# Kernel tuning notes

Measured on AMD Instinct MI355X. Metric: run time of the kernel, lower is better.

The kernel has to match this reference:

```python
import jax, jax.numpy as jnp
import numpy as np

N, E, D, H, O, L = 50000, 400000, 128, 128, 64, 2


def setup_inputs() -> dict:
    key = jax.random.key(0)
    ks = jax.random.split(key, 24)
    s = 0.05
    rn = lambda k, shape: jax.random.normal(k, shape, jnp.float32) * s
    # random edges with no self-loops (dst = src + nonzero offset mod N)
    src = jax.random.randint(ks[0], (E,), 0, N, dtype=jnp.int32)
    off = jax.random.randint(ks[1], (E,), 1, N, dtype=jnp.int32)
    dst = (src + off) % N
    edge_index = jnp.stack([src, dst])  # [2, E] int32
    return {
        "x": rn(ks[2], (N, D)),
        "edge_index": edge_index,
        "attn_W": rn(ks[3], (L, 2 * D, 2)),
        "attn_b": rn(ks[4], (L, 2)),
        "mlp_W1": rn(ks[5], (L, D, H)),
        "mlp_b1": rn(ks[6], (L, H)),
        "mlp_W2": rn(ks[7], (L, H, H)),
        "mlp_b2": rn(ks[8], (L, H)),
        "bn_gamma": jnp.ones((L, H), jnp.float32),   # torch BatchNorm1d default affine init
        "bn_beta": jnp.zeros((L, H), jnp.float32),
        "gru_Wih": rn(ks[9], (D, 3 * H)),
        "gru_Whh": rn(ks[10], (H, 3 * H)),
        "gru_bih": rn(ks[11], (3 * H,)),
        "gru_bhh": rn(ks[12], (3 * H,)),
        "last_W1": rn(ks[13], (H, H)),
        "last_b1": rn(ks[14], (H,)),
        "last_W2": rn(ks[15], (H, O)),
        "last_b2": rn(ks[16], (O,)),
    }


def reference(x, edge_index, attn_W, attn_b, mlp_W1, mlp_b1, mlp_W2, mlp_b2,
              bn_gamma, bn_beta, gru_Wih, gru_Whh, gru_bih, gru_bhh,
              last_W1, last_b1, last_W2, last_b2):
    n = x.shape[0]
    # symmetrize edge list: message (nbr -> node) for both directions
    node = jnp.concatenate([edge_index[0], edge_index[1]])  # destination
    nbr = jnp.concatenate([edge_index[1], edge_index[0]])   # source / neighbor
    deg = jax.ops.segment_sum(jnp.ones((node.shape[0], 1), x.dtype), node, num_segments=n)
    has_nbr = deg > 0

    h_state = jnp.zeros((n, gru_Whh.shape[0]), x.dtype)
    for l in range(attn_W.shape[0]):
        feats = x[nbr]  # [2E, d] gather
        s_agg = jax.ops.segment_sum(feats, node, num_segments=n)
        m_agg = jax.ops.segment_max(feats, node, num_segments=n)
        m_agg = jnp.where(has_nbr, m_agg, jnp.zeros_like(m_agg))  # isolated nodes stay 0
        # attention over {sum, max} aggregations
        scores = jnp.concatenate([s_agg, m_agg], axis=1) @ attn_W[l] + attn_b[l]  # [n, 2]
        w = jax.nn.softmax(scores, axis=1)
        comb = x + w[:, :1] * s_agg + w[:, 1:] * m_agg
        # MLP (in -> hidden, ReLU, hidden -> out)
        z = jax.nn.relu(comb @ mlp_W1[l] + mlp_b1[l]) @ mlp_W2[l] + mlp_b2[l]
        # BatchNorm1d in eval mode with running stats (mean 0, var 1): affine only
        z = z * bn_gamma[l] + bn_beta[l]
        # GRUCell
        gi = z @ gru_Wih + gru_bih
        gh = h_state @ gru_Whh + gru_bhh
        ir, iz, inn = jnp.split(gi, 3, axis=1)
        hr, hz, hn = jnp.split(gh, 3, axis=1)
        r = jax.nn.sigmoid(ir + hr)
        u = jax.nn.sigmoid(iz + hz)
        ncand = jnp.tanh(inn + r * hn)
        h_state = (1.0 - u) * ncand + u * h_state
        x = h_state
    # final node-level MLP
    out = jax.nn.relu(x @ last_W1 + last_b1) @ last_W2 + last_b2
    return out
```

## Files before the change

### kernel.cpp

```cpp
#include <hip/hip_runtime.h>
#include <math.h>

typedef unsigned short u16;
typedef __attribute__((ext_vector_type(8))) short bf16x8;
typedef __attribute__((ext_vector_type(4))) float f32x4;

#define ADJ_CAP 96

__device__ __forceinline__ u16 f2b(float f) {
    union { float f; unsigned u; } v; v.f = f;
    unsigned r = (v.u + 0x7FFF + ((v.u >> 16) & 1)) >> 16;
    return (u16)r;
}
__device__ __forceinline__ float b2f(u16 h) {
    union { unsigned u; float f; } v; v.u = (unsigned)h << 16;
    return v.f;
}
__device__ __forceinline__ float u2f(unsigned u) {
    union { unsigned u; float f; } v; v.u = u;
    return v.f;
}
__device__ __forceinline__ float fsig(float x) { return 1.f / (1.f + __expf(-x)); }
__device__ __forceinline__ float ftanh(float x) {
    float e = __expf(2.f * x);
    return 1.f - 2.f / (e + 1.f);
}

__device__ __forceinline__ void gll16(const void* g, void* l) {
    __builtin_amdgcn_global_load_lds(
        (const __attribute__((address_space(1))) void*)g,
        (__attribute__((address_space(3))) void*)l, 16, 0, 0);
}

__device__ __forceinline__ void conv_chunk(const float* __restrict__ src,
                                           u16* __restrict__ dst, int c, int NC) {
    int sl = c / NC, n = c - sl * NC;
    u16 tmp[8];
#pragma unroll
    for (int i = 0; i < 8; ++i) tmp[i] = f2b(src[(size_t)(sl * 8 + i) * NC + n]);
    *(uint4*)(dst + (size_t)c * 8) = *(const uint4*)tmp;
}

__global__ void k_pro(const int* __restrict__ ei, int* __restrict__ cnt,
                      u16* __restrict__ adj, int E, int N,
                      const float* __restrict__ W1, const float* __restrict__ W2,
                      const float* __restrict__ Wih, const float* __restrict__ Whh,
                      const float* __restrict__ lW1, const float* __restrict__ lW2,
                      u16* __restrict__ tW1, u16* __restrict__ tW2,
                      u16* __restrict__ tGRU,
                      u16* __restrict__ tlW1, u16* __restrict__ tlW2, int L,
                      const float* __restrict__ x, u16* __restrict__ xb, int n8) {
    const int EB = (E + 255) >> 8;
    const int nwc = L * 4096 + 12288 + 3072;
    const int WB = (nwc + 255) >> 8;
    int b = blockIdx.x;
    if (b < EB * 8) {
        const int part = b & 7, chunk = b >> 3;
        const int span = (N + 7) >> 3;
        const int nlo = part * span;
        const int nhi = (nlo + span < N) ? nlo + span : N;
        int e = chunk * 256 + threadIdx.x;
        if (e < E) {
            int s = ei[e], d = ei[E + e];
            if (s >= nlo && s < nhi) {
                int p = atomicAdd(&cnt[s], 1);
                adj[(size_t)s * ADJ_CAP + p] = (u16)d;
            }
            if (d >= nlo && d < nhi) {
                int q = atomicAdd(&cnt[d], 1);
                adj[(size_t)d * ADJ_CAP + q] = (u16)s;
            }
        }
        return;
    }
    b -= EB * 8;
    if (b < WB) {
        int c = b * 256 + threadIdx.x;
        if (c >= nwc) return;
        if (c < L * 2048) { int l = c >> 11; conv_chunk(W1 + (size_t)l * 16384, tW1 + (size_t)l * 16384, c & 2047, 128); return; }
        c -= L * 2048;
        if (c < L * 2048) { int l = c >> 11; conv_chunk(W2 + (size_t)l * 16384, tW2 + (size_t)l * 16384, c & 2047, 128); return; }
        c -= L * 2048;
        if (c < 12288) {
            int s = c >> 9, r = c & 511;
            int q = r >> 7, mat = (r >> 6) & 1, cc = r & 63;
            int h = s / 12, s2 = s % 12, kc = s2 / 3, g = s2 % 3;
            int ocol = g * 128 + h * 64 + cc;
            const float* src = mat ? Whh : Wih;
            int kb = (kc * 4 + q) * 8;
            u16 tmp[8];
#pragma unroll
            for (int e = 0; e < 8; ++e) tmp[e] = f2b(src[(size_t)(kb + e) * 384 + ocol]);
            *(uint4*)(tGRU + (size_t)c * 8) = *(const uint4*)tmp;
            return;
        }
        c -= 12288;
        if (c < 2048) { conv_chunk(lW1, tlW1, c, 128); return; }
        c -= 2048;
        if (c < 1024) { conv_chunk(lW2, tlW2, c, 64); return; }
        return;
    }
    b -= WB;
    {
        int i = b * 256 + threadIdx.x;
        if (i < n8) {
            float4 a = *(const float4*)(x + (size_t)i * 8);
            float4 bb = *(const float4*)(x + (size_t)i * 8 + 4);
            u16 t[8] = {f2b(a.x), f2b(a.y), f2b(a.z), f2b(a.w),
                        f2b(bb.x), f2b(bb.y), f2b(bb.z), f2b(bb.w)};
            *(uint4*)(xb + (size_t)i * 8) = *(const uint4*)t;
        }
    }
}

__global__ __launch_bounds__(256) void k_agg(const u16* __restrict__ xb,
                                             const u16* __restrict__ adj,
                                             const int* __restrict__ cnt,
                                             const float* __restrict__ aW,
                                             const float* __restrict__ ab,
                                             u16* __restrict__ comb, int N) {
    int n = blockIdx.x * 4 + (threadIdx.x >> 6);
    if (n >= N) return;
    int l = threadIdx.x & 63;
    int grp = l >> 4;
    int f0 = (l & 15) * 8;
    int beg = n * ADJ_CAP, deg = cnt[n], end = beg + deg;
    float s[8], m[8];
#pragma unroll
    for (int i = 0; i < 8; ++i) { s[i] = 0.f; m[i] = -3.402823e38f; }

    auto acc8 = [&](uint4 v) {
        unsigned d[4] = {v.x, v.y, v.z, v.w};
#pragma unroll
        for (int i = 0; i < 4; ++i) {
            float a0 = u2f(d[i] << 16);
            float a1 = u2f(d[i] & 0xFFFF0000u);
            s[2 * i] += a0;     m[2 * i] = fmaxf(m[2 * i], a0);
            s[2 * i + 1] += a1; m[2 * i + 1] = fmaxf(m[2 * i + 1], a1);
        }
    };

    int j = beg + grp;
    for (; j + 4 < end; j += 8) {
        int a0 = adj[j], a1 = adj[j + 4];
        uint4 v0 = *(const uint4*)(xb + (size_t)a0 * 128 + f0);
        uint4 v1 = *(const uint4*)(xb + (size_t)a1 * 128 + f0);
        acc8(v0);
        acc8(v1);
    }
    if (j < end) {
        int a = adj[j];
        uint4 v = *(const uint4*)(xb + (size_t)a * 128 + f0);
        acc8(v);
    }
#pragma unroll
    for (int i = 0; i < 8; ++i) {
        s[i] += __shfl_xor(s[i], 16);
        s[i] += __shfl_xor(s[i], 32);
        m[i] = fmaxf(m[i], __shfl_xor(m[i], 16));
        m[i] = fmaxf(m[i], __shfl_xor(m[i], 32));
    }
    if (deg == 0) {
#pragma unroll
        for (int i = 0; i < 8; ++i) m[i] = 0.f;
    }
    float p0 = 0.f, p1 = 0.f;
#pragma unroll
    for (int i = 0; i < 8; ++i) {
        float2 wS = *(const float2*)(aW + (size_t)(f0 + i) * 2);
        float2 wM = *(const float2*)(aW + (size_t)(128 + f0 + i) * 2);
        p0 += s[i] * wS.x + m[i] * wM.x;
        p1 += s[i] * wS.y + m[i] * wM.y;
    }
#pragma unroll
    for (int o = 8; o; o >>= 1) { p0 += __shfl_xor(p0, o); p1 += __shfl_xor(p1, o); }
    p0 += ab[0]; p1 += ab[1];
    float pm = fmaxf(p0, p1);
    float ea = __expf(p0 - pm), eb = __expf(p1 - pm);
    float w0 = ea / (ea + eb), w1 = 1.f - w0;
    if (grp == 0) {
        uint4 xv = *(const uint4*)(xb + (size_t)n * 128 + f0);
        unsigned xs[4] = {xv.x, xv.y, xv.z, xv.w};
        unsigned dw[4];
#pragma unroll
        for (int i = 0; i < 4; ++i) {
            float xlo = u2f(xs[i] << 16), xhi = u2f(xs[i] & 0xFFFF0000u);
            float olo = xlo + w0 * s[2 * i] + w1 * m[2 * i];
            float ohi = xhi + w0 * s[2 * i + 1] + w1 * m[2 * i + 1];
            dw[i] = (unsigned)f2b(olo) | ((unsigned)f2b(ohi) << 16);
        }
        uint4 o4 = make_uint4(dw[0], dw[1], dw[2], dw[3]);
        *(uint4*)(comb + (size_t)n * 128 + f0) = o4;
    }
}

template <bool H0, bool FIN>
__global__ __launch_bounds__(256, 4) void k_layer(
    const u16* __restrict__ Cb, const u16* __restrict__ Hb,
    const u16* __restrict__ W1t, const float* __restrict__ b1,
    const u16* __restrict__ W2t, const float* __restrict__ b2,
    const float* __restrict__ gam, const float* __restrict__ bet,
    const u16* __restrict__ tG,
    const float* __restrict__ bih, const float* __restrict__ bhh,
    u16* __restrict__ HnB,
    const u16* __restrict__ lW1t, const float* __restrict__ lb1,
    const u16* __restrict__ lW2t, const float* __restrict__ lb2,
    float* __restrict__ out, int M) {
    __shared__ __align__(16) u16 x_s[64 * 16 * 8];
    __shared__ __align__(16) u16 b_s[3][4096];
    const int t = threadIdx.x;
    const int m0 = blockIdx.x * 64;
    const int wid = t >> 6, lane = t & 63, lo = lane & 15, hi = lane >> 4;
    const int arow = 16 * wid + lo;
    const int LAST = FIN ? 37 : 31;

    auto issue = [&](int s) {
        const u16* g;
        if (s < 4)                 g = W1t + (size_t)s * 4096;
        else if (s < 8)            g = W2t + (size_t)(s - 4) * 4096;
        else if (!FIN || s < 32)   g = tG + (size_t)(s - 8) * 4096;
        else if (s < 36)           g = lW1t + (size_t)(s - 32) * 4096;
        else                       g = lW2t + (size_t)(s - 36) * 4096;
        char* l = (char*)b_s[s % 3] + wid * 2048;
        const char* gp = (const char*)g + wid * 2048 + lane * 16;
        gll16(gp, l);
        gll16(gp + 1024, l + 1024);
    };

    float b1r[8], g2r[8], t2r[8];
#pragma unroll
    for (int j = 0; j < 8; ++j) {
        int c = 16 * j + lo;
        b1r[j] = b1[c];
        float gv = gam[c];
        g2r[j] = gv;
        t2r[j] = b2[c] * gv + bet[c];
    }
#pragma unroll
    for (int i = 0; i < 4; ++i) {
        int off = (i * 4 + wid) * 1024;
        int row = (off >> 8) + (lane >> 4);
        int sl = lane & 15;
        int gr = m0 + row; gr = gr < M ? gr : M - 1;
        gll16(Cb + (size_t)gr * 128 + ((sl ^ (row & 7)) * 8), (char*)x_s + off);
    }
    issue(0);
    issue(1);

    f32x4 acc[8];
#pragma unroll
    for (int j = 0; j < 8; ++j) acc[j] = (f32x4)0.f;

#pragma unroll
    for (int ks = 0; ks < 4; ++ks) {
        const int p = ks;
        asm volatile("s_waitcnt vmcnt(2)" ::: "memory");
        __builtin_amdgcn_s_barrier();
        issue(p + 2);
        bf16x8 af = *(const bf16x8*)&x_s[(arow * 16 + ((ks * 4 + hi) ^ (arow & 7))) * 8];
        const u16* buf = b_s[p % 3];
        __builtin_amdgcn_s_setprio(1);
#pragma unroll
        for (int j = 0; j < 8; ++j) {
            bf16x8 bf = *(const bf16x8*)&buf[((size_t)hi * 128 + 16 * j + lo) * 8];
            acc[j] = __builtin_amdgcn_mfma_f32_16x16x32_bf16(af, bf, acc[j], 0, 0, 0);
        }
        __builtin_amdgcn_s_setprio(0);
    }
#pragma unroll
    for (int j = 0; j < 8; ++j) {
        int c = 16 * j + lo;
#pragma unroll
        for (int q = 0; q < 4; ++q) {
            int row = 16 * wid + hi * 4 + q;
            float v = fmaxf(acc[j][q] + b1r[j], 0.f);
            int sl = c >> 3;
            x_s[(row * 16 + (sl ^ (row & 7))) * 8 + (c & 7)] = f2b(v);
        }
        acc[j] = (f32x4)0.f;
    }

#pragma unroll
    for (int ks = 0; ks < 4; ++ks) {
        const int p = 4 + ks;
        asm volatile("s_waitcnt vmcnt(2)" ::: "memory");
        __builtin_amdgcn_s_barrier();
        issue(p + 2);
        bf16x8 af = *(const bf16x8*)&x_s[(arow * 16 + ((ks * 4 + hi) ^ (arow & 7))) * 8];
        const u16* buf = b_s[p % 3];
        __builtin_amdgcn_s_setprio(1);
#pragma unroll
        for (int j = 0; j < 8; ++j) {
            bf16x8 bf = *(const bf16x8*)&buf[((size_t)hi * 128 + 16 * j + lo) * 8];
            acc[j] = __builtin_amdgcn_mfma_f32_16x16x32_bf16(af, bf, acc[j], 0, 0, 0);
        }
        __builtin_amdgcn_s_setprio(0);
    }
#pragma unroll
    for (int j = 0; j < 8; ++j) {
        int c = 16 * j + lo;
#pragma unroll
        for (int q = 0; q < 4; ++q) {
            int row = 16 * wid + hi * 4 + q;
            float v = acc[j][q] * g2r[j] + t2r[j];
            int sl = c >> 3;
            x_s[(row * 16 + (sl ^ (row & 7))) * 8 + (c & 7)] = f2b(v);
        }
    }
    bf16x8 hreg[4];
    if (!H0) {
        int gr = m0 + arow; gr = gr < M ? gr : M - 1;
#pragma unroll
        for (int kc = 0; kc < 4; ++kc)
            hreg[kc] = *(const bf16x8*)(Hb + (size_t)gr * 128 + (kc * 4 + hi) * 8);
    }

    f32x4 racc[4], uacc[4], nza[4], nha[4];
    float o_all[2][4][4];

    auto epi = [&](int h, float (&oo)[4][4]) {
#pragma unroll
        for (int ct = 0; ct < 4; ++ct) {
            int c = h * 64 + ct * 16 + lo;
            float b_r = bih[c] + bhh[c];
            float b_u = bih[c + 128] + bhh[c + 128];
            float b_in = bih[c + 256], b_hn = bhh[c + 256];
#pragma unroll
            for (int q = 0; q < 4; ++q) {
                int r = m0 + 16 * wid + hi * 4 + q;
                float o = 0.f;
                if (r < M) {
                    float rr = fsig(racc[ct][q] + b_r);
                    float uu = fsig(uacc[ct][q] + b_u);
                    float hterm = H0 ? b_hn : (nha[ct][q] + b_hn);
                    float nn = ftanh(nza[ct][q] + b_in + rr * hterm);
                    float hv = H0 ? 0.f : b2f(Hb[(size_t)r * 128 + c]);
                    o = (1.f - uu) * nn + uu * hv;
                    if (!FIN) HnB[(size_t)r * 128 + c] = f2b(o);
                }
                if (FIN) oo[ct][q] = o;
            }
        }
    };

#pragma unroll
    for (int h = 0; h < 2; ++h) {
#pragma unroll
        for (int j = 0; j < 4; ++j) {
            racc[j] = (f32x4)0.f; uacc[j] = (f32x4)0.f;
            nza[j] = (f32x4)0.f; nha[j] = (f32x4)0.f;
        }
#pragma unroll
        for (int kc = 0; kc < 4; ++kc) {
            bf16x8 zf;
#pragma unroll
            for (int g = 0; g < 3; ++g) {
                const int p = 8 + h * 12 + kc * 3 + g;
                if (!FIN && p == 31) asm volatile("s_waitcnt vmcnt(0)" ::: "memory");
                else                 asm volatile("s_waitcnt vmcnt(2)" ::: "memory");
                __builtin_amdgcn_s_barrier();
                if (p + 2 <= LAST) issue(p + 2);
                if (g == 0)
                    zf = *(const bf16x8*)&x_s[(arow * 16 + ((kc * 4 + hi) ^ (arow & 7))) * 8];
                const u16* buf = b_s[p % 3];
                __builtin_amdgcn_s_setprio(1);
#pragma unroll
                for (int jj = 0; jj < 4; ++jj) {
                    bf16x8 wi = *(const bf16x8*)&buf[((size_t)hi * 128 + jj * 16 + lo) * 8];
                    if (g == 0)      racc[jj] = __builtin_amdgcn_mfma_f32_16x16x32_bf16(zf, wi, racc[jj], 0, 0, 0);
                    else if (g == 1) uacc[jj] = __builtin_amdgcn_mfma_f32_16x16x32_bf16(zf, wi, uacc[jj], 0, 0, 0);
                    else             nza[jj]  = __builtin_amdgcn_mfma_f32_16x16x32_bf16(zf, wi, nza[jj], 0, 0, 0);
                    if (!H0) {
                        bf16x8 wh = *(const bf16x8*)&buf[((size_t)hi * 128 + 64 + jj * 16 + lo) * 8];
                        if (g == 0)      racc[jj] = __builtin_amdgcn_mfma_f32_16x16x32_bf16(hreg[kc], wh, racc[jj], 0, 0, 0);
                        else if (g == 1) uacc[jj] = __builtin_amdgcn_mfma_f32_16x16x32_bf16(hreg[kc], wh, uacc[jj], 0, 0, 0);
                        else             nha[jj]  = __builtin_amdgcn_mfma_f32_16x16x32_bf16(hreg[kc], wh, nha[jj], 0, 0, 0);
                    }
                }
                __builtin_amdgcn_s_setprio(0);
            }
        }
        epi(h, o_all[h]);
    }

    if (FIN) {
#pragma unroll
        for (int h = 0; h < 2; ++h)
#pragma unroll
            for (int ct = 0; ct < 4; ++ct) {
                int c = h * 64 + ct * 16 + lo;
#pragma unroll
                for (int q = 0; q < 4; ++q) {
                    int row = 16 * wid + hi * 4 + q;
                    int sl = c >> 3;
                    x_s[(row * 16 + (sl ^ (row & 7))) * 8 + (c & 7)] = f2b(o_all[h][ct][q]);
                }
            }
#pragma unroll
        for (int j = 0; j < 8; ++j) acc[j] = (f32x4)0.f;
#pragma unroll
        for (int ks = 0; ks < 4; ++ks) {
            const int p = 32 + ks;
            asm volatile("s_waitcnt vmcnt(2)" ::: "memory");
            __builtin_amdgcn_s_barrier();
            if (p + 2 <= 37) issue(p + 2);
            bf16x8 af = *(const bf16x8*)&x_s[(arow * 16 + ((ks * 4 + hi) ^ (arow & 7))) * 8];
            const u16* buf = b_s[p % 3];
            __builtin_amdgcn_s_setprio(1);
#pragma unroll
            for (int j = 0; j < 8; ++j) {
                bf16x8 bf = *(const bf16x8*)&buf[((size_t)hi * 128 + 16 * j + lo) * 8];
                acc[j] = __builtin_amdgcn_mfma_f32_16x16x32_bf16(af, bf, acc[j], 0, 0, 0);
            }
            __builtin_amdgcn_s_setprio(0);
        }
#pragma unroll
        for (int j = 0; j < 8; ++j) {
            int c = 16 * j + lo;
            float bv = lb1[c];
#pragma unroll
            for (int q = 0; q < 4; ++q) {
                int row = 16 * wid + hi * 4 + q;
                float v = fmaxf(acc[j][q] + bv, 0.f);
                int sl = c >> 3;
                x_s[(row * 16 + (sl ^ (row & 7))) * 8 + (c & 7)] = f2b(v);
            }
        }
        f32x4 a2[4];
#pragma unroll
        for (int j = 0; j < 4; ++j) a2[j] = (f32x4)0.f;
#pragma unroll
        for (int ph = 0; ph < 2; ++ph) {
            const int p = 36 + ph;
            if (p == 37) asm volatile("s_waitcnt vmcnt(0)" ::: "memory");
            else         asm volatile("s_waitcnt vmcnt(2)" ::: "memory");
            __builtin_amdgcn_s_barrier();
            const u16* buf = b_s[p % 3];
            __builtin_amdgcn_s_setprio(1);
#pragma unroll
            for (int k2 = 0; k2 < 2; ++k2) {
                int ks = ph * 2 + k2;
                bf16x8 af = *(const bf16x8*)&x_s[(arow * 16 + ((ks * 4 + hi) ^ (arow & 7))) * 8];
                int lk = k2 * 4 + hi;
#pragma unroll
                for (int jj = 0; jj < 4; ++jj) {
                    bf16x8 bf = *(const bf16x8*)&buf[((size_t)lk * 64 + 16 * jj + lo) * 8];
                    a2[jj] = __builtin_amdgcn_mfma_f32_16x16x32_bf16(af, bf, a2[jj], 0, 0, 0);
                }
            }
            __builtin_amdgcn_s_setprio(0);
        }
#pragma unroll
        for (int jj = 0; jj < 4; ++jj) {
            int c = 16 * jj + lo;
            float bv = lb2[c];
#pragma unroll
            for (int q = 0; q < 4; ++q) {
                int r = m0 + 16 * wid + hi * 4 + q;
                if (r < M) out[(size_t)r * 64 + c] = a2[jj][q] + bv;
            }
        }
    }
}

extern "C" void kernel_launch(void* const* d_in, const int* in_sizes, int n_in,
                              void* d_out, int out_size, void* d_ws, size_t ws_size,
                              hipStream_t stream) {
    const float* x   = (const float*)d_in[0];
    const int*   ei  = (const int*)d_in[1];
    const float* aW  = (const float*)d_in[2];
    const float* ab  = (const float*)d_in[3];
    const float* W1  = (const float*)d_in[4];
    const float* b1  = (const float*)d_in[5];
    const float* W2  = (const float*)d_in[6];
    const float* b2  = (const float*)d_in[7];
    const float* gam = (const float*)d_in[8];
    const float* bet = (const float*)d_in[9];
    const float* Wih = (const float*)d_in[10];
    const float* Whh = (const float*)d_in[11];
    const float* bih = (const float*)d_in[12];
    const float* bhh = (const float*)d_in[13];
    const float* lW1 = (const float*)d_in[14];
    const float* lb1 = (const float*)d_in[15];
    const float* lW2 = (const float*)d_in[16];
    const float* lb2 = (const float*)d_in[17];

    const int N = in_sizes[0] / 128;
    const int E = in_sizes[1] / 2;
    const int L = in_sizes[3] / 2;
    float* out = (float*)d_out;

    char* ws = (char*)d_ws;
    size_t off = 0;
    auto alloc = [&](size_t bytes) -> void* {
        void* p = ws + off;
        off = (off + bytes + 255) & ~(size_t)255;
        return p;
    };
    int* cnt  = (int*)alloc((size_t)N * 4);
    u16* adj  = (u16*)alloc((size_t)N * ADJ_CAP * 2);
    u16* tW1  = (u16*)alloc((size_t)L * 16384 * 2);
    u16* tW2  = (u16*)alloc((size_t)L * 16384 * 2);
    u16* tGRU = (u16*)alloc((size_t)98304 * 2);
    u16* tlW1 = (u16*)alloc((size_t)16384 * 2);
    u16* tlW2 = (u16*)alloc((size_t)8192 * 2);
    u16* xb   = (u16*)alloc((size_t)N * 128 * 2);
    u16* comb = (u16*)alloc((size_t)N * 128 * 2);
    u16* hAb  = (u16*)alloc((size_t)N * 128 * 2);
    (void)ws_size; (void)n_in; (void)out_size;

    hipMemsetAsync(cnt, 0, (size_t)N * 4, stream);

    const int EB = (E + 255) / 256;
    const int nwc = L * 4096 + 12288 + 3072;
    const int WB = (nwc + 255) / 256;
    const int FB = (N * 16 + 255) / 256;
    k_pro<<<EB * 8 + WB + FB, 256, 0, stream>>>(ei, cnt, adj, E, N,
                                                W1, W2, Wih, Whh, lW1, lW2,
                                                tW1, tW2, tGRU, tlW1, tlW2, L,
                                                x, xb, N * 16);

    const int mb = (N + 63) / 64;
    k_agg<<<(N + 3) / 4, 256, 0, stream>>>(xb, adj, cnt, aW, ab, comb, N);
    k_layer<true, false><<<mb, 256, 0, stream>>>(
        comb, nullptr, tW1, b1, tW2, b2, gam, bet,
        tGRU, bih, bhh, hAb,
        nullptr, nullptr, nullptr, nullptr, nullptr, N);
    k_agg<<<(N + 3) / 4, 256, 0, stream>>>(hAb, adj, cnt, aW + 512, ab + 2, comb, N);
    k_layer<false, true><<<mb, 256, 0, stream>>>(
        comb, hAb, tW1 + 16384, b1 + 128, tW2 + 16384, b2 + 128,
        gam + 128, bet + 128, tGRU, bih, bhh, nullptr,
        tlW1, lb1, tlW2, lb2, out, N);
}
```

Baseline: 245.0 us.

## Double layer tile to 128 rows and split final MLP into separate kernel

The fused layer kernel now uses 512-thread blocks covering 128 rows, so each staged weight chunk is shared by twice as many rows, and each thread issues one async load per stage instead of two. The final node MLP is taken out of the second layer kernel and run as a separate k_final kernel, which reads the hidden state from a new workspace buffer. The edge-index reads in the prologue use nontemporal loads. In exchange, the extra kernel launch and the hidden-state round trip through global memory add traffic, and the larger blocks may reduce occupancy.

```diff
diff --git a/kernel.cpp b/kernel.cpp
--- a/kernel.cpp
+++ b/kernel.cpp
@@ -61,7 +61,8 @@
         const int nhi = (nlo + span < N) ? nlo + span : N;
         int e = chunk * 256 + threadIdx.x;
         if (e < E) {
-            int s = ei[e], d = ei[E + e];
+            int s = __builtin_nontemporal_load(&ei[e]);
+            int d = __builtin_nontemporal_load(&ei[E + e]);
             if (s >= nlo && s < nhi) {
                 int p = atomicAdd(&cnt[s], 1);
                 adj[(size_t)s * ADJ_CAP + p] = (u16)d;
@@ -194,37 +195,29 @@
     }
 }
 
-template <bool H0, bool FIN>
-__global__ __launch_bounds__(256, 4) void k_layer(
+template <bool H0>
+__global__ __launch_bounds__(512, 4) void k_layer(
     const u16* __restrict__ Cb, const u16* __restrict__ Hb,
     const u16* __restrict__ W1t, const float* __restrict__ b1,
     const u16* __restrict__ W2t, const float* __restrict__ b2,
     const float* __restrict__ gam, const float* __restrict__ bet,
     const u16* __restrict__ tG,
     const float* __restrict__ bih, const float* __restrict__ bhh,
-    u16* __restrict__ HnB,
-    const u16* __restrict__ lW1t, const float* __restrict__ lb1,
-    const u16* __restrict__ lW2t, const float* __restrict__ lb2,
-    float* __restrict__ out, int M) {
-    __shared__ __align__(16) u16 x_s[64 * 16 * 8];
+    u16* __restrict__ HnB, int M) {
+    __shared__ __align__(16) u16 x_s[128 * 16 * 8];
     __shared__ __align__(16) u16 b_s[3][4096];
     const int t = threadIdx.x;
-    const int m0 = blockIdx.x * 64;
+    const int m0 = blockIdx.x * 128;
     const int wid = t >> 6, lane = t & 63, lo = lane & 15, hi = lane >> 4;
     const int arow = 16 * wid + lo;
-    const int LAST = FIN ? 37 : 31;
 
     auto issue = [&](int s) {
-        const u16* g;
-        if (s < 4)                 g = W1t + (size_t)s * 4096;
-        else if (s < 8)            g = W2t + (size_t)(s - 4) * 4096;
-        else if (!FIN || s < 32)   g = tG + (size_t)(s - 8) * 4096;
-        else if (s < 36)           g = lW1t + (size_t)(s - 32) * 4096;
-        else                       g = lW2t + (size_t)(s - 36) * 4096;
-        char* l = (char*)b_s[s % 3] + wid * 2048;
-        const char* gp = (const char*)g + wid * 2048 + lane * 16;
+        const u16* g = (s < 4) ? (W1t + (size_t)s * 4096)
+                     : (s < 8) ? (W2t + (size_t)(s - 4) * 4096)
+                               : (tG + (size_t)(s - 8) * 4096);
+        char* l = (char*)b_s[s % 3] + wid * 1024;
+        const char* gp = (const char*)g + wid * 1024 + lane * 16;
         gll16(gp, l);
-        gll16(gp + 1024, l + 1024);
     };
 
     float b1r[8], g2r[8], t2r[8];
@@ -238,7 +231,7 @@
     }
 #pragma unroll
     for (int i = 0; i < 4; ++i) {
-        int off = (i * 4 + wid) * 1024;
+        int off = (i * 8 + wid) * 1024;
         int row = (off >> 8) + (lane >> 4);
         int sl = lane & 15;
         int gr = m0 + row; gr = gr < M ? gr : M - 1;
@@ -254,7 +247,7 @@
 #pragma unroll
     for (int ks = 0; ks < 4; ++ks) {
         const int p = ks;
-        asm volatile("s_waitcnt vmcnt(2)" ::: "memory");
+        asm volatile("s_waitcnt vmcnt(1)" ::: "memory");
         __builtin_amdgcn_s_barrier();
         issue(p + 2);
         bf16x8 af = *(const bf16x8*)&x_s[(arow * 16 + ((ks * 4 + hi) ^ (arow & 7))) * 8];
@@ -283,7 +276,7 @@
 #pragma unroll
     for (int ks = 0; ks < 4; ++ks) {
         const int p = 4 + ks;
-        asm volatile("s_waitcnt vmcnt(2)" ::: "memory");
+        asm volatile("s_waitcnt vmcnt(1)" ::: "memory");
         __builtin_amdgcn_s_barrier();
         issue(p + 2);
         bf16x8 af = *(const bf16x8*)&x_s[(arow * 16 + ((ks * 4 + hi) ^ (arow & 7))) * 8];
@@ -316,9 +309,8 @@
     }
 
     f32x4 racc[4], uacc[4], nza[4], nha[4];
-    float o_all[2][4][4];
-
-    auto epi = [&](int h, float (&oo)[4][4]) {
+
+    auto epi = [&](int h) {
 #pragma unroll
         for (int ct = 0; ct < 4; ++ct) {
             int c = h * 64 + ct * 16 + lo;
@@ -328,17 +320,15 @@
 #pragma unroll
             for (int q = 0; q < 4; ++q) {
                 int r = m0 + 16 * wid + hi * 4 + q;
-                float o = 0.f;
                 if (r < M) {
                     float rr = fsig(racc[ct][q] + b_r);
                     float uu = fsig(uacc[ct][q] + b_u);
                     float hterm = H0 ? b_hn : (nha[ct][q] + b_hn);
                     float nn = ftanh(nza[ct][q] + b_in + rr * hterm);
                     float hv = H0 ? 0.f : b2f(Hb[(size_t)r * 128 + c]);
-                    o = (1.f - uu) * nn + uu * hv;
-                    if (!FIN) HnB[(size_t)r * 128 + c] = f2b(o);
+                    float o = (1.f - uu) * nn + uu * hv;
+                    HnB[(size_t)r * 128 + c] = f2b(o);
                 }
-                if (FIN) oo[ct][q] = o;
             }
         }
     };
@@ -356,10 +346,10 @@
 #pragma unroll
             for (int g = 0; g < 3; ++g) {
                 const int p = 8 + h * 12 + kc * 3 + g;
-                if (!FIN && p == 31) asm volatile("s_waitcnt vmcnt(0)" ::: "memory");
-                else                 asm volatile("s_waitcnt vmcnt(2)" ::: "memory");
+                if (p == 31) asm volatile("s_waitcnt vmcnt(0)" ::: "memory");
+                else         asm volatile("s_waitcnt vmcnt(1)" ::: "memory");
                 __builtin_amdgcn_s_barrier();
-                if (p + 2 <= LAST) issue(p + 2);
+                if (p + 2 <= 31) issue(p + 2);
                 if (g == 0)
                     zf = *(const bf16x8*)&x_s[(arow * 16 + ((kc * 4 + hi) ^ (arow & 7))) * 8];
                 const u16* buf = b_s[p % 3];
@@ -380,85 +370,87 @@
                 __builtin_amdgcn_s_setprio(0);
             }
         }
-        epi(h, o_all[h]);
-    }
-
-    if (FIN) {
-#pragma unroll
-        for (int h = 0; h < 2; ++h)
-#pragma unroll
-            for (int ct = 0; ct < 4; ++ct) {
-                int c = h * 64 + ct * 16 + lo;
-#pragma unroll
-                for (int q = 0; q < 4; ++q) {
-                    int row = 16 * wid + hi * 4 + q;
-                    int sl = c >> 3;
-                    x_s[(row * 16 + (sl ^ (row & 7))) * 8 + (c & 7)] = f2b(o_all[h][ct][q]);
-                }
-            }
-#pragma unroll
-        for (int j = 0; j < 8; ++j) acc[j] = (f32x4)0.f;
-#pragma unroll
-        for (int ks = 0; ks < 4; ++ks) {
-            const int p = 32 + ks;
-            asm volatile("s_waitcnt vmcnt(2)" ::: "memory");
-            __builtin_amdgcn_s_barrier();
-            if (p + 2 <= 37) issue(p + 2);
-            bf16x8 af = *(const bf16x8*)&x_s[(arow * 16 + ((ks * 4 + hi) ^ (arow & 7))) * 8];
-            const u16* buf = b_s[p % 3];
-            __builtin_amdgcn_s_setprio(1);
-#pragma unroll
-            for (int j = 0; j < 8; ++j) {
-                bf16x8 bf = *(const bf16x8*)&buf[((size_t)hi * 128 + 16 * j + lo) * 8];
-                acc[j] = __builtin_amdgcn_mfma_f32_16x16x32_bf16(af, bf, acc[j], 0, 0, 0);
-            }
-            __builtin_amdgcn_s_setprio(0);
-        }
+        epi(h);
+    }
+}
+
+__global__ __launch_bounds__(256, 2) void k_final(const u16* __restrict__ Hb,
+                                                  const u16* __restrict__ W1t,
+                                                  const float* __restrict__ b1,
+                                                  const u16* __restrict__ W2t,
+                                                  const float* __restrict__ b2,
+                                                  float* __restrict__ out, int M) {
+    __shared__ __align__(16) u16 x_s[64 * 16 * 8];
+    __shared__ __align__(16) u16 w_s[16 * 128 * 8];
+    const int t = threadIdx.x;
+    const int m0 = blockIdx.x * 64;
+    const int w = t >> 6, l = t & 63, lo = l & 15, hi = l >> 4;
+    const int arow = 16 * w + lo;
+#pragma unroll
+    for (int i = 0; i < 4; ++i) {
+        int idx = t + i * 256;
+        int row = idx >> 4, sl = idx & 15;
+        int gr = m0 + row; gr = gr < M ? gr : M - 1;
+        *(uint4*)&x_s[(row * 16 + (sl ^ (row & 7))) * 8] =
+            *(const uint4*)(Hb + (size_t)gr * 128 + sl * 8);
+    }
+#pragma unroll
+    for (int i = 0; i < 8; ++i) {
+        int idx = t + i * 256;
+        *(uint4*)&w_s[idx * 8] = *(const uint4*)(W1t + (size_t)idx * 8);
+    }
+    __syncthreads();
+    f32x4 acc[8];
+#pragma unroll
+    for (int j = 0; j < 8; ++j) acc[j] = (f32x4)0.f;
+#pragma unroll
+    for (int ks = 0; ks < 4; ++ks) {
+        bf16x8 af = *(const bf16x8*)&x_s[(arow * 16 + ((ks * 4 + hi) ^ (arow & 7))) * 8];
 #pragma unroll
         for (int j = 0; j < 8; ++j) {
-            int c = 16 * j + lo;
-            float bv = lb1[c];
-#pragma unroll
-            for (int q = 0; q < 4; ++q) {
-                int row = 16 * wid + hi * 4 + q;
-                float v = fmaxf(acc[j][q] + bv, 0.f);
-                int sl = c >> 3;
-                x_s[(row * 16 + (sl ^ (row & 7))) * 8 + (c & 7)] = f2b(v);
-            }
-        }
-        f32x4 a2[4];
-#pragma unroll
-        for (int j = 0; j < 4; ++j) a2[j] = (f32x4)0.f;
-#pragma unroll
-        for (int ph = 0; ph < 2; ++ph) {
-            const int p = 36 + ph;
-            if (p == 37) asm volatile("s_waitcnt vmcnt(0)" ::: "memory");
-            else         asm volatile("s_waitcnt vmcnt(2)" ::: "memory");
-            __builtin_amdgcn_s_barrier();
-            const u16* buf = b_s[p % 3];
-            __builtin_amdgcn_s_setprio(1);
-#pragma unroll
-            for (int k2 = 0; k2 < 2; ++k2) {
-                int ks = ph * 2 + k2;
-                bf16x8 af = *(const bf16x8*)&x_s[(arow * 16 + ((ks * 4 + hi) ^ (arow & 7))) * 8];
-                int lk = k2 * 4 + hi;
-#pragma unroll
-                for (int jj = 0; jj < 4; ++jj) {
-                    bf16x8 bf = *(const bf16x8*)&buf[((size_t)lk * 64 + 16 * jj + lo) * 8];
-                    a2[jj] = __builtin_amdgcn_mfma_f32_16x16x32_bf16(af, bf, a2[jj], 0, 0, 0);
-                }
-            }
-            __builtin_amdgcn_s_setprio(0);
-        }
-#pragma unroll
-        for (int jj = 0; jj < 4; ++jj) {
-            int c = 16 * jj + lo;
-            float bv = lb2[c];
-#pragma unroll
-            for (int q = 0; q < 4; ++q) {
-                int r = m0 + 16 * wid + hi * 4 + q;
-                if (r < M) out[(size_t)r * 64 + c] = a2[jj][q] + bv;
-            }
+            bf16x8 bf = *(const bf16x8*)&w_s[((ks * 4 + hi) * 128 + 16 * j + lo) * 8];
+            acc[j] = __builtin_amdgcn_mfma_f32_16x16x32_bf16(af, bf, acc[j], 0, 0, 0);
+        }
+    }
+    __syncthreads();
+#pragma unroll
+    for (int j = 0; j < 8; ++j) {
+        int c = 16 * j + lo;
+        float bv = b1[c];
+#pragma unroll
+        for (int q = 0; q < 4; ++q) {
+            int row = 16 * w + hi * 4 + q;
+            float v = fmaxf(acc[j][q] + bv, 0.f);
+            int sl = c >> 3;
+            x_s[(row * 16 + (sl ^ (row & 7))) * 8 + (c & 7)] = f2b(v);
+        }
+    }
+#pragma unroll
+    for (int i = 0; i < 4; ++i) {
+        int idx = t + i * 256;
+        *(uint4*)&w_s[idx * 8] = *(const uint4*)(W2t + (size_t)idx * 8);
+    }
+    __syncthreads();
+    f32x4 a2[4];
+#pragma unroll
+    for (int j = 0; j < 4; ++j) a2[j] = (f32x4)0.f;
+#pragma unroll
+    for (int ks = 0; ks < 4; ++ks) {
+        bf16x8 af = *(const bf16x8*)&x_s[(arow * 16 + ((ks * 4 + hi) ^ (arow & 7))) * 8];
+#pragma unroll
+        for (int j = 0; j < 4; ++j) {
+            bf16x8 bf = *(const bf16x8*)&w_s[((ks * 4 + hi) * 64 + 16 * j + lo) * 8];
+            a2[j] = __builtin_amdgcn_mfma_f32_16x16x32_bf16(af, bf, a2[j], 0, 0, 0);
+        }
+    }
+#pragma unroll
+    for (int j = 0; j < 4; ++j) {
+        int c = 16 * j + lo;
+        float bv = b2[c];
+#pragma unroll
+        for (int q = 0; q < 4; ++q) {
+            int r = m0 + 16 * w + hi * 4 + q;
+            if (r < M) out[(size_t)r * 64 + c] = a2[j][q] + bv;
         }
     }
 }
@@ -507,6 +499,7 @@
     u16* xb   = (u16*)alloc((size_t)N * 128 * 2);
     u16* comb = (u16*)alloc((size_t)N * 128 * 2);
     u16* hAb  = (u16*)alloc((size_t)N * 128 * 2);
+    u16* hBb  = (u16*)alloc((size_t)N * 128 * 2);
     (void)ws_size; (void)n_in; (void)out_size;
 
     hipMemsetAsync(cnt, 0, (size_t)N * 4, stream);
@@ -520,15 +513,15 @@
                                                 tW1, tW2, tGRU, tlW1, tlW2, L,
                                                 x, xb, N * 16);
 
-    const int mb = (N + 63) / 64;
+    const int mb = (N + 127) / 128;
     k_agg<<<(N + 3) / 4, 256, 0, stream>>>(xb, adj, cnt, aW, ab, comb, N);
-    k_layer<true, false><<<mb, 256, 0, stream>>>(
+    k_layer<true><<<mb, 512, 0, stream>>>(
         comb, nullptr, tW1, b1, tW2, b2, gam, bet,
-        tGRU, bih, bhh, hAb,
-        nullptr, nullptr, nullptr, nullptr, nullptr, N);
+        tGRU, bih, bhh, hAb, N);
     k_agg<<<(N + 3) / 4, 256, 0, stream>>>(hAb, adj, cnt, aW + 512, ab + 2, comb, N);
-    k_layer<false, true><<<mb, 256, 0, stream>>>(
+    k_layer<false><<<mb, 512, 0, stream>>>(
         comb, hAb, tW1 + 16384, b1 + 128, tW2 + 16384, b2 + 128,
-        gam + 128, bet + 128, tGRU, bih, bhh, nullptr,
-        tlW1, lb1, tlW2, lb2, out, N);
-}
+        gam + 128, bet + 128, tGRU, bih, bhh, hBb, N);
+
+    k_final<<<(N + 63) / 64, 256, 0, stream>>>(hBb, tlW1, lb1, tlW2, lb2, out, N);
+}
```

After: 222.0 us. 1.1x faster.
